# Optimization experiments

Hardware: AMD Instinct MI355X
Metric: run time of the kernel (lower is better)

The kernel has to match this reference:

```python
import jax, jax.numpy as jnp
import numpy as np

N = 5000
NFEAT = 512
NHID = 64
NHEADS = 8
NCLASS = 40
ALPHA = 0.2  # leaky relu slope
NEG_INF = -9e15


def setup_inputs() -> dict:
    key = jax.random.key(0)
    ks = jax.random.split(key, 12)
    x = jax.random.normal(ks[0], (N, NFEAT), dtype=jnp.float32)
    # binary adjacency, ~32 avg degree, with self loops
    adj = (jax.random.uniform(ks[1], (N, N)) < (32.0 / N)).astype(jnp.float32)
    adj = jnp.maximum(adj, jnp.eye(N, dtype=jnp.float32))
    s = 1.0 / np.sqrt(NFEAT)
    W_h = jax.random.uniform(ks[2], (NHEADS, NFEAT, NHID), minval=-s, maxval=s, dtype=jnp.float32)
    a_h = jax.random.uniform(ks[3], (NHEADS, 2 * NHID), minval=-s, maxval=s, dtype=jnp.float32)
    s2 = 1.0 / np.sqrt(NHID * NHEADS)
    W_o = jax.random.uniform(ks[4], (NHID * NHEADS, NHID), minval=-s2, maxval=s2, dtype=jnp.float32)
    a_o = jax.random.uniform(ks[5], (2 * NHID,), minval=-s2, maxval=s2, dtype=jnp.float32)
    s3 = 1.0 / np.sqrt(NHID)
    fc1_w = jax.random.uniform(ks[6], (NHID, 200), minval=-s3, maxval=s3, dtype=jnp.float32)
    fc1_b = jax.random.uniform(ks[7], (200,), minval=-s3, maxval=s3, dtype=jnp.float32)
    s4 = 1.0 / np.sqrt(200)
    fc2_w = jax.random.uniform(ks[8], (200, NCLASS), minval=-s4, maxval=s4, dtype=jnp.float32)
    fc2_b = jax.random.uniform(ks[9], (NCLASS,), minval=-s4, maxval=s4, dtype=jnp.float32)
    return {"x": x, "adj": adj, "W_h": W_h, "a_h": a_h, "W_o": W_o, "a_o": a_o,
            "fc1_w": fc1_w, "fc1_b": fc1_b, "fc2_w": fc2_w, "fc2_b": fc2_b}


def _masked_attention(e, adj):
    # e: [..., N, N]; mask where adj == 0, then row softmax
    e = jnp.where(adj > 0, e, NEG_INF)
    return jax.nn.softmax(e, axis=-1)


def reference(x, adj, W_h, a_h, W_o, a_o, fc1_w, fc1_b, fc2_w, fc2_b):
    # ---- multi-head GAT layer (concat=True), eval mode (dropout off) ----
    Wh = jnp.einsum('nf,hfo->hno', x, W_h)                 # [H, N, nhid]
    f1 = jnp.einsum('hno,ho->hn', Wh, a_h[:, :NHID])       # [H, N]
    f2 = jnp.einsum('hno,ho->hn', Wh, a_h[:, NHID:])       # [H, N]
    e = jax.nn.leaky_relu(f1[:, :, None] + f2[:, None, :], ALPHA)  # [H, N, N]
    att = _masked_attention(e, adj[None, :, :])
    h = jnp.einsum('hnm,hmo->hno', att, Wh)                # [H, N, nhid]
    h1 = jax.nn.elu(h).transpose(1, 0, 2).reshape(N, NHEADS * NHID)  # concat heads

    # ---- output GAT layer (concat=False) ----
    Wh2 = h1 @ W_o                                         # [N, nhid]
    g1 = Wh2 @ a_o[:NHID]                                  # [N]
    g2 = Wh2 @ a_o[NHID:]                                  # [N]
    e2 = jax.nn.leaky_relu(g1[:, None] + g2[None, :], ALPHA)
    att2 = _masked_attention(e2, adj)
    h2 = att2 @ Wh2                                        # [N, nhid]

    # ---- MLP head ----
    h3 = jax.nn.elu(h2 @ fc1_w + fc1_b)
    return h3 @ fc2_w + fc2_b                              # [N, nclass]
```

## Files before the change

kernel.cpp:

```cpp
#include <hip/hip_runtime.h>

typedef unsigned short u16;
typedef unsigned int u32;
typedef unsigned long long u64;
typedef __bf16 bf16_t;
typedef __bf16 bf16x8 __attribute__((ext_vector_type(8)));
typedef u16 u16x8 __attribute__((ext_vector_type(8)));
typedef float f32x4 __attribute__((ext_vector_type(4)));
typedef u32 u32x4 __attribute__((ext_vector_type(4)));

#define NN 5000
#define NF 512
#define NH 64
#define HEADS 8
#define NCLS 40
#define CAP 128
#define LRELU 0.2f

#define BM_BLKS 1250
#define G1_BLKS (79 * HEADS)
#define K1_GRID (BM_BLKS + G1_BLKS)
#define W0_BLKS 64
#define PRM_BLKS 8
#define K0_GRID (W0_BLKS + PRM_BLKS)

__device__ __forceinline__ bool adj_is_bf16(const void* adj) {
    return ((*(const u32*)adj) & 0xFFFFu) != 0u;
}
__device__ __forceinline__ u16 rne_bf16(float f) {
    u32 u = __float_as_uint(f);
    u += 0x7FFFu + ((u >> 16) & 1u);
    return (u16)(u >> 16);
}
__device__ __forceinline__ float up_bf16(u16 h) {
    return __uint_as_float((u32)h << 16);
}
__device__ __forceinline__ float in_f32(const void* p, int idx, bool isb) {
    return isb ? up_bf16(((const u16*)p)[idx]) : ((const float*)p)[idx];
}
__device__ __forceinline__ u32x4 ntload4(const void* p, int idx) {
    return __builtin_nontemporal_load(((const u32x4*)p) + idx);
}
union U8cast { u16x8 u; bf16x8 b; };

__global__ __launch_bounds__(256) void cvt_w(const void* __restrict__ W_h,
                                             const void* __restrict__ adj,
                                             const void* W_o, const void* a_o,
                                             const void* f1w, const void* f1b,
                                             const void* f2w, const void* f2b,
                                             u16* __restrict__ whc,
                                             float* W_oc, float* a_oc,
                                             float* f1wc, float* f1bc,
                                             float* f2wc, float* f2bc) {
    const bool isb = adj_is_bf16(adj);
    const int b = blockIdx.x;
    if (b < W0_BLKS) {
        const int W4 = HEADS * NF * NH / 4;
        for (int iw = b * 256 + threadIdx.x; iw < W4; iw += W0_BLKS * 256) {
            u16 q[4];
            if (isb) {
                ushort4 vv = ((const ushort4*)W_h)[iw];
                q[0] = vv.x; q[1] = vv.y; q[2] = vv.z; q[3] = vv.w;
            } else {
                u32x4 vv = ntload4(W_h, iw);
                q[0] = rne_bf16(__uint_as_float(vv[0])); q[1] = rne_bf16(__uint_as_float(vv[1]));
                q[2] = rne_bf16(__uint_as_float(vv[2])); q[3] = rne_bf16(__uint_as_float(vv[3]));
            }
            const int e0 = iw * 4;
            const int h = e0 >> 15;
            const int rem = e0 & 32767;
            const int f = rem >> 6, o0 = rem & 63;
            const int base = (h * 16 + (f >> 5)) * 2048 + ((f >> 3) & 3) * 128 + (f & 7);
            #pragma unroll
            for (int k = 0; k < 4; ++k) {
                const int o = o0 + k;
                whc[base + (o >> 4) * 512 + (o & 15) * 8] = q[k];
            }
        }
    } else {
        const int s1 = HEADS * NH * NH, s2 = 2 * NH,
                  s3 = NH * 200, s4 = 200, s5 = 200 * NCLS, s6 = NCLS;
        const int total = s1 + s2 + s3 + s4 + s5 + s6;
        const int pb = b - W0_BLKS;
        for (int i = pb * 256 + threadIdx.x; i < total; i += PRM_BLKS * 256) {
            const void* src; float* dst; int off = i;
            if (off < s1) { src = W_o;  dst = W_oc; }
            else if ((off -= s1) < s2) { src = a_o;  dst = a_oc; }
            else if ((off -= s2) < s3) { src = f1w;  dst = f1wc; }
            else if ((off -= s3) < s4) { src = f1b;  dst = f1bc; }
            else if ((off -= s4) < s5) { src = f2w;  dst = f2wc; }
            else { off -= s5;           src = f2b;  dst = f2bc; }
            dst[off] = isb ? up_bf16(((const u16*)src)[off]) : ((const float*)src)[off];
        }
    }
}

__global__ __launch_bounds__(256) void gemm1_f(const void* __restrict__ x,
                                               const bf16_t* __restrict__ Wf,
                                               const void* __restrict__ a_h,
                                               const void* __restrict__ adj,
                                               int* __restrict__ nbr, int* __restrict__ deg,
                                               float* __restrict__ Wh,
                                               float* __restrict__ f1,
                                               float* __restrict__ f2) {
    const bool isb = adj_is_bf16(adj);
    const int lane = threadIdx.x & 63;
    const int wid  = threadIdx.x >> 6;
    const int b = blockIdx.x;

    int aidx = -1, gidx = -1;
    if (b < 1875) {
        const int g = b / 3, r3 = b % 3;
        if (r3 < 2) aidx = 2 * g + r3;
        else        gidx = g;
    } else {
        gidx = 625 + (b - 1875);
    }

    if (aidx >= 0) {
        const int r = aidx * 4 + wid;
        u64 my0 = 0ull, my1 = 0ull;
        if (!isb) {
            const float* row = (const float*)adj + (size_t)r * NN;
            #pragma unroll
            for (int pass = 0; pass < 2; ++pass) {
                u32x4 v[10];
                #pragma unroll
                for (int k = 0; k < 10; ++k) {
                    int c = (pass * 10 + k) * 64 + lane;
                    v[k] = (c < 1250) ? ntload4(row, c) : (u32x4){0u, 0u, 0u, 0u};
                }
                #pragma unroll
                for (int k = 0; k < 10; ++k) {
                    int i = pass * 10 + k;
                    #pragma unroll
                    for (int j = 0; j < 4; ++j) {
                        u64 m = __ballot(v[k][j] != 0u);
                        int w = i * 4 + j;
                        if (w == lane)      my0 = m;
                        if (w == lane + 64) my1 = m;
                    }
                }
            }
        } else {
            const u16* row = (const u16*)adj + (size_t)r * NN;
            u32x4 v[10];
            #pragma unroll
            for (int k = 0; k < 10; ++k) {
                int c = k * 64 + lane;
                v[k] = (c < 625) ? ntload4(row, c) : (u32x4){0u, 0u, 0u, 0u};
            }
            #pragma unroll
            for (int k = 0; k < 10; ++k) {
                #pragma unroll
                for (int j = 0; j < 4; ++j) {
                    u64 mlo = __ballot((v[k][j] & 0xFFFFu) != 0u);
                    u64 mhi = __ballot((v[k][j] >> 16) != 0u);
                    int wl = k * 8 + 2 * j, wh = wl + 1;
                    if (wl == lane)      my0 = mlo;
                    if (wl == lane + 64) my1 = mlo;
                    if (wh == lane)      my0 = mhi;
                    if (wh == lane + 64) my1 = mhi;
                }
            }
        }
        int* nrow = nbr + (size_t)r * CAP;
        int pc = __popcll(my0);
        int scan = pc;
        #pragma unroll
        for (int o = 1; o < 64; o <<= 1) {
            int t2 = __shfl_up(scan, o);
            if (lane >= o) scan += t2;
        }
        int off = scan - pc;
        {
            const int w = lane;
            u64 mw = my0;
            while (mw) {
                int bb = __ffsll(mw) - 1;
                mw &= mw - 1;
                int elem = !isb ? ((w >> 2) * 64 + bb) * 4 + (w & 3)
                                : ((w >> 3) * 64 + bb) * 8 + (w & 7);
                if (off < CAP) nrow[off] = elem;
                ++off;
            }
        }
        const int base = __shfl(scan, 63);
        int pc1 = __popcll(my1);
        int scan1 = pc1;
        #pragma unroll
        for (int o = 1; o < 64; o <<= 1) {
            int t2 = __shfl_up(scan1, o);
            if (lane >= o) scan1 += t2;
        }
        int off1 = base + scan1 - pc1;
        {
            const int w = lane + 64;
            u64 mw = my1;
            while (mw) {
                int bb = __ffsll(mw) - 1;
                mw &= mw - 1;
                int elem = !isb ? ((w >> 2) * 64 + bb) * 4 + (w & 3)
                                : ((w >> 3) * 64 + bb) * 8 + (w & 7);
                if (off1 < CAP) nrow[off1] = elem;
                ++off1;
            }
        }
        const int total = base + __shfl(scan1, 63);
        if (lane == 0) deg[r] = total < CAP ? total : CAP;
        return;
    }

    const int rg = gidx % 79;
    const int h  = gidx / 79;
    const int quad = lane >> 4;
    const int lr   = lane & 15;
    const int kq   = quad * 8;
    const int nCol = wid * 16 + lr;
    __shared__ float f1s[4][64], f2s[4][64];

    const bf16_t* Bf = Wf + (size_t)h * (16 * 2048) + threadIdx.x * 8;
    bf16x8 bfrag[16];
    #pragma unroll
    for (int s = 0; s < 16; ++s) bfrag[s] = *(const bf16x8*)(Bf + s * 2048);

    const float a1c = in_f32(a_h, h * 128 + nCol, isb);
    const float a2c = in_f32(a_h, h * 128 + NH + nCol, isb);

    for (int t = 0; t < 4; ++t) {
        const int rb = rg * 64 + t * 16;
        int row  = rb + lr;
        int rowc = row < NN ? row : NN - 1;
        f32x4 acc = {0.f, 0.f, 0.f, 0.f};
        if (!isb) {
            const float* xp = (const float*)x + (size_t)rowc * NF + kq;
            #pragma unroll
            for (int s = 0; s < 16; ++s) {
                float4 lo = *(const float4*)(xp + s * 32);
                float4 hi = *(const float4*)(xp + s * 32 + 4);
                bf16x8 a;
                a[0] = (bf16_t)lo.x; a[1] = (bf16_t)lo.y; a[2] = (bf16_t)lo.z; a[3] = (bf16_t)lo.w;
                a[4] = (bf16_t)hi.x; a[5] = (bf16_t)hi.y; a[6] = (bf16_t)hi.z; a[7] = (bf16_t)hi.w;
                acc = __builtin_amdgcn_mfma_f32_16x16x32_bf16(a, bfrag[s], acc, 0, 0, 0);
            }
        } else {
            const u16* xp = (const u16*)x + (size_t)rowc * NF + kq;
            #pragma unroll
            for (int s = 0; s < 16; ++s) {
                U8cast cc;
                cc.u = *(const u16x8*)(xp + s * 32);
                acc = __builtin_amdgcn_mfma_f32_16x16x32_bf16(cc.b, bfrag[s], acc, 0, 0, 0);
            }
        }
        #pragma unroll
        for (int r = 0; r < 4; ++r) {
            int gr = rb + quad * 4 + r;
            if (gr < NN) Wh[(size_t)gr * (HEADS * NH) + h * NH + nCol] = acc[r];
            float p1 = acc[r] * a1c, p2 = acc[r] * a2c;
            #pragma unroll
            for (int o = 8; o; o >>= 1) { p1 += __shfl_xor(p1, o); p2 += __shfl_xor(p2, o); }
            if (lr == 0) { f1s[wid][t * 16 + quad * 4 + r] = p1; f2s[wid][t * 16 + quad * 4 + r] = p2; }
        }
    }
    __syncthreads();
    if (wid == 0) {
        int gr = rg * 64 + lane;
        if (gr < NN) {
            f1[h * NN + gr] = f1s[0][lane] + f1s[1][lane] + f1s[2][lane] + f1s[3][lane];
            f2[h * NN + gr] = f2s[0][lane] + f2s[1][lane] + f2s[2][lane] + f2s[3][lane];
        }
    }
}

__global__ __launch_bounds__(256) void agg1f(const int* __restrict__ nbr,
                                             const int* __restrict__ deg,
                                             const float* __restrict__ Wh,
                                             const float* __restrict__ f1,
                                             const float* __restrict__ f2,
                                             float* __restrict__ h1) {
    const int lane = threadIdx.x & 63;
    const int wid  = threadIdx.x >> 6;
    const int n = blockIdx.x;
    __shared__ int s_nbr[CAP];
    __shared__ float s_p[8][CAP];
    const int d = deg[n];
    for (int i = threadIdx.x; i < d; i += 256) s_nbr[i] = nbr[(size_t)n * CAP + i];
    __syncthreads();

    const int ha = wid, hb = wid + 4;
    const int nb0 = (lane < d) ? s_nbr[lane] : 0;
    const int nb1 = (lane + 64 < d) ? s_nbr[lane + 64] : 0;
    const float f10 = f1[ha * NN + n], f11 = f1[hb * NN + n];
    const float* f2ha = f2 + (size_t)ha * NN;
    const float* f2hb = f2 + (size_t)hb * NN;

    float e00 = -INFINITY, e01 = -INFINITY, e10 = -INFINITY, e11 = -INFINITY;
    if (lane < d) {
        float a = f10 + f2ha[nb0]; e00 = a > 0.f ? a : LRELU * a;
        float b = f11 + f2hb[nb0]; e10 = b > 0.f ? b : LRELU * b;
    }
    if (lane + 64 < d) {
        float a = f10 + f2ha[nb1]; e01 = a > 0.f ? a : LRELU * a;
        float b = f11 + f2hb[nb1]; e11 = b > 0.f ? b : LRELU * b;
    }
    float mx0 = fmaxf(e00, e01), mx1 = fmaxf(e10, e11);
    #pragma unroll
    for (int o = 32; o; o >>= 1) {
        mx0 = fmaxf(mx0, __shfl_xor(mx0, o));
        mx1 = fmaxf(mx1, __shfl_xor(mx1, o));
    }
    float p00 = lane < d ? expf(e00 - mx0) : 0.f;
    float p01 = lane + 64 < d ? expf(e01 - mx0) : 0.f;
    float p10 = lane < d ? expf(e10 - mx1) : 0.f;
    float p11 = lane + 64 < d ? expf(e11 - mx1) : 0.f;
    float sm0 = p00 + p01, sm1 = p10 + p11;
    #pragma unroll
    for (int o = 32; o; o >>= 1) { sm0 += __shfl_xor(sm0, o); sm1 += __shfl_xor(sm1, o); }

    const float i0 = 1.f / sm0, i1 = 1.f / sm1;
    s_p[ha][lane] = p00 * i0; s_p[ha][lane + 64] = p01 * i0;
    s_p[hb][lane] = p10 * i1; s_p[hb][lane + 64] = p11 * i1;
    __syncthreads();

    const float* ap = s_p[2 * wid + (lane >> 5)];
    const float* wp = Wh + wid * 128 + 2 * lane;
    float A0x = 0.f, A0y = 0.f, A1x = 0.f, A1y = 0.f;
    float A2x = 0.f, A2y = 0.f, A3x = 0.f, A3y = 0.f;
    int j = 0;
    for (; j + 8 <= d; j += 8) {
        #pragma unroll
        for (int u = 0; u < 8; ++u) {
            const float2 v = *(const float2*)(wp + (size_t)s_nbr[j + u] * (HEADS * NH));
            const float a = ap[j + u];
            if ((u & 3) == 0)      { A0x += a * v.x; A0y += a * v.y; }
            else if ((u & 3) == 1) { A1x += a * v.x; A1y += a * v.y; }
            else if ((u & 3) == 2) { A2x += a * v.x; A2y += a * v.y; }
            else                   { A3x += a * v.x; A3y += a * v.y; }
        }
    }
    for (; j < d; ++j) {
        const float2 v = *(const float2*)(wp + (size_t)s_nbr[j] * (HEADS * NH));
        const float a = ap[j];
        A0x += a * v.x; A0y += a * v.y;
    }
    float hx = A0x + A1x + A2x + A3x;
    float hy = A0y + A1y + A2y + A3y;
    hx = hx > 0.f ? hx : expf(hx) - 1.f;
    hy = hy > 0.f ? hy : expf(hy) - 1.f;
    *(float2*)(h1 + (size_t)n * (HEADS * NH) + wid * 128 + 2 * lane) = make_float2(hx, hy);
}

__global__ __launch_bounds__(256) void gemm2_4(const float* __restrict__ h1,
                                               const float* __restrict__ W_o,
                                               const float* __restrict__ a_o,
                                               float* __restrict__ Wh2,
                                               float* __restrict__ g1,
                                               float* __restrict__ g2) {
    const int t = threadIdx.x;
    const int n0 = blockIdx.x * 4;
    __shared__ float sh[4 * 512];
    __shared__ float ps[4][4][64];
    const float4* src = (const float4*)(h1 + (size_t)n0 * 512);
    ((float4*)sh)[t]       = src[t];
    ((float4*)sh)[t + 256] = src[t + 256];
    __syncthreads();
    const int o = t & 63, part = t >> 6;
    float a0 = 0.f, a1 = 0.f, a2 = 0.f, a3 = 0.f;
    const float* wo = W_o + part * 128 * 64 + o;
    const float* s0 = sh + part * 128;
    #pragma unroll 4
    for (int f = 0; f < 128; ++f) {
        float w = wo[f * 64];
        a0 += s0[f] * w; a1 += s0[512 + f] * w; a2 += s0[1024 + f] * w; a3 += s0[1536 + f] * w;
    }
    ps[part][0][o] = a0; ps[part][1][o] = a1; ps[part][2][o] = a2; ps[part][3][o] = a3;
    __syncthreads();
    const int nd = t >> 6;
    float w2 = ps[0][nd][o] + ps[1][nd][o] + ps[2][nd][o] + ps[3][nd][o];
    Wh2[(size_t)(n0 + nd) * 64 + o] = w2;
    float p1 = w2 * a_o[o], p2 = w2 * a_o[64 + o];
    #pragma unroll
    for (int s = 32; s; s >>= 1) { p1 += __shfl_xor(p1, s); p2 += __shfl_xor(p2, s); }
    if (o == 0) { g1[n0 + nd] = p1; g2[n0 + nd] = p2; }
}

__global__ __launch_bounds__(256) void agg2_mlp(const float* __restrict__ Wh2,
                                                const float* __restrict__ g1,
                                                const float* __restrict__ g2,
                                                const int* __restrict__ nbr,
                                                const int* __restrict__ deg,
                                                const float* __restrict__ fc1_w,
                                                const float* __restrict__ fc1_b,
                                                const float* __restrict__ fc2_w,
                                                const float* __restrict__ fc2_b,
                                                float* __restrict__ out) {
    const int lane = threadIdx.x & 63;
    const int wid  = threadIdx.x >> 6;
    const int t = threadIdx.x;
    const int n0 = blockIdx.x * 4;
    const int n = n0 + wid;
    __shared__ float s_alpha[4][CAP];
    __shared__ int   s_nbr[4][CAP];
    __shared__ float s_h2[4][NH];
    __shared__ float s_h3[4][200];
    __shared__ float ps2[2][4][NCLS];
    const int d = deg[n];
    const int* nb = nbr + (size_t)n * CAP;
    const float gn = g1[n];

    float mx = -INFINITY;
    for (int j = lane; j < d; j += 64) {
        int m = nb[j];
        s_nbr[wid][j] = m;
        float e = gn + g2[m];
        e = e > 0.f ? e : LRELU * e;
        s_alpha[wid][j] = e;
        mx = fmaxf(mx, e);
    }
    #pragma unroll
    for (int o = 32; o; o >>= 1) mx = fmaxf(mx, __shfl_xor(mx, o));
    float sm = 0.f;
    for (int j = lane; j < d; j += 64) {
        float p = expf(s_alpha[wid][j] - mx);
        s_alpha[wid][j] = p;
        sm += p;
    }
    #pragma unroll
    for (int o = 32; o; o >>= 1) sm += __shfl_xor(sm, o);

    float acc0 = 0.f, acc1 = 0.f, acc2 = 0.f, acc3 = 0.f;
    int j = 0;
    for (; j + 4 <= d; j += 4) {
        acc0 += s_alpha[wid][j]     * Wh2[(size_t)s_nbr[wid][j]     * NH + lane];
        acc1 += s_alpha[wid][j + 1] * Wh2[(size_t)s_nbr[wid][j + 1] * NH + lane];
        acc2 += s_alpha[wid][j + 2] * Wh2[(size_t)s_nbr[wid][j + 2] * NH + lane];
        acc3 += s_alpha[wid][j + 3] * Wh2[(size_t)s_nbr[wid][j + 3] * NH + lane];
    }
    for (; j < d; ++j) acc0 += s_alpha[wid][j] * Wh2[(size_t)s_nbr[wid][j] * NH + lane];
    s_h2[wid][lane] = (acc0 + acc1 + acc2 + acc3) / sm;
    __syncthreads();

    if (t < 200) {
        float b0 = 0.f, b1 = 0.f, b2 = 0.f, b3 = 0.f;
        #pragma unroll 4
        for (int f = 0; f < NH; ++f) {
            float w = fc1_w[f * 200 + t];
            b0 += s_h2[0][f] * w; b1 += s_h2[1][f] * w; b2 += s_h2[2][f] * w; b3 += s_h2[3][f] * w;
        }
        float bb = fc1_b[t];
        b0 += bb; b1 += bb; b2 += bb; b3 += bb;
        s_h3[0][t] = b0 > 0.f ? b0 : expf(b0) - 1.f;
        s_h3[1][t] = b1 > 0.f ? b1 : expf(b1) - 1.f;
        s_h3[2][t] = b2 > 0.f ? b2 : expf(b2) - 1.f;
        s_h3[3][t] = b3 > 0.f ? b3 : expf(b3) - 1.f;
    }
    __syncthreads();

    if (t < 80) {
        const int o = t % 40, fh = t / 40;
        float c0 = 0.f, c1 = 0.f, c2 = 0.f, c3 = 0.f;
        #pragma unroll 4
        for (int f = fh * 100; f < fh * 100 + 100; ++f) {
            float w = fc2_w[f * NCLS + o];
            c0 += s_h3[0][f] * w; c1 += s_h3[1][f] * w; c2 += s_h3[2][f] * w; c3 += s_h3[3][f] * w;
        }
        ps2[fh][0][o] = c0; ps2[fh][1][o] = c1; ps2[fh][2][o] = c2; ps2[fh][3][o] = c3;
    }
    __syncthreads();
    if (t < 160) {
        const int nd = t / 40, o = t % 40;
        out[(size_t)(n0 + nd) * NCLS + o] = ps2[0][nd][o] + ps2[1][nd][o] + fc2_b[o];
    }
}

extern "C" void kernel_launch(void* const* d_in, const int* in_sizes, int n_in,
                              void* d_out, int out_size, void* d_ws, size_t ws_size,
                              hipStream_t stream) {
    const void* x     = d_in[0];
    const void* adj   = d_in[1];
    const void* W_h   = d_in[2];
    const void* a_h   = d_in[3];
    const void* W_o   = d_in[4];
    const void* a_o   = d_in[5];
    const void* fc1_w = d_in[6];
    const void* fc1_b = d_in[7];
    const void* fc2_w = d_in[8];
    const void* fc2_b = d_in[9];
    float* out = (float*)d_out;

    char* ws = (char*)d_ws;
    int*   nbr   = (int*)(ws + 0);
    int*   deg   = (int*)(ws + 2560000);
    float* Wh    = (float*)(ws + 2580000);
    float* f1    = (float*)(ws + 12820000);
    float* f2    = (float*)(ws + 12980000);
    float* h1    = (float*)(ws + 13140000);
    float* Wh2   = (float*)(ws + 23380000);
    float* g1    = (float*)(ws + 24660000);
    float* g2    = (float*)(ws + 24680000);
    float* W_oc  = (float*)(ws + 24700000);
    float* a_oc  = (float*)(ws + 24831072);
    float* f1wc  = (float*)(ws + 24831584);
    float* f1bc  = (float*)(ws + 24882784);
    float* f2wc  = (float*)(ws + 24883584);
    float* f2bc  = (float*)(ws + 24915584);
    u16*   whc   = (u16*)(ws + 24915744);

    cvt_w<<<K0_GRID, 256, 0, stream>>>(W_h, adj, W_o, a_o, fc1_w, fc1_b, fc2_w, fc2_b,
                                       whc, W_oc, a_oc, f1wc, f1bc, f2wc, f2bc);
    gemm1_f<<<K1_GRID, 256, 0, stream>>>(x, (const bf16_t*)whc, a_h, adj,
                                         nbr, deg, Wh, f1, f2);
    agg1f<<<NN, 256, 0, stream>>>(nbr, deg, Wh, f1, f2, h1);
    gemm2_4<<<NN / 4, 256, 0, stream>>>(h1, W_oc, a_oc, Wh2, g1, g2);
    agg2_mlp<<<NN / 4, 256, 0, stream>>>(Wh2, g1, g2, nbr, deg,
                                         f1wc, f1bc, f2wc, f2bc, out);
}
```

Before: 301.8 us.

## Split adjacency row scan across two waves and reorder GEMM-first block layout

The adjacency-to-neighbor-list pass now assigns each row to two waves, each scanning half the columns. Their counts are combined through shared memory and a block barrier, where before one wave made two passes over the whole row. The adjacency blocks now come after the GEMM blocks in the grid instead of being interleaved in a 2:1 pattern. The aim is more memory-level parallelism and shorter per-wave latency on the bandwidth-bound adjacency read, at the cost of a __syncthreads and twice as many adjacency blocks.

```diff
diff --git a/kernel.cpp b/kernel.cpp
--- a/kernel.cpp
+++ b/kernel.cpp
@@ -17,9 +17,9 @@
 #define CAP 128
 #define LRELU 0.2f
 
-#define BM_BLKS 1250
 #define G1_BLKS (79 * HEADS)
-#define K1_GRID (BM_BLKS + G1_BLKS)
+#define ADJ_BLKS 2500
+#define K1_GRID (G1_BLKS + ADJ_BLKS)
 #define W0_BLKS 64
 #define PRM_BLKS 8
 #define K0_GRID (W0_BLKS + PRM_BLKS)
@@ -103,121 +103,91 @@
                                                float* __restrict__ Wh,
                                                float* __restrict__ f1,
                                                float* __restrict__ f2) {
-    const bool isb = adj_is_bf16(adj);
     const int lane = threadIdx.x & 63;
     const int wid  = threadIdx.x >> 6;
     const int b = blockIdx.x;
-
-    int aidx = -1, gidx = -1;
-    if (b < 1875) {
-        const int g = b / 3, r3 = b % 3;
-        if (r3 < 2) aidx = 2 * g + r3;
-        else        gidx = g;
-    } else {
-        gidx = 625 + (b - 1875);
-    }
-
-    if (aidx >= 0) {
-        const int r = aidx * 4 + wid;
-        u64 my0 = 0ull, my1 = 0ull;
+    __shared__ float f1s[4][64], f2s[4][64];
+    __shared__ int s_cnt[4];
+
+    if (b >= G1_BLKS) {
+        const bool isb = adj_is_bf16(adj);
+        const int a = b - G1_BLKS;
+        const int r = a * 2 + (wid >> 1);
+        const int hf = wid & 1;
+        u64 myw = 0ull;
         if (!isb) {
             const float* row = (const float*)adj + (size_t)r * NN;
-            #pragma unroll
-            for (int pass = 0; pass < 2; ++pass) {
-                u32x4 v[10];
+            u32x4 v[10];
+            #pragma unroll
+            for (int k = 0; k < 10; ++k) {
+                int c = hf * 640 + k * 64 + lane;
+                v[k] = (c < 1250) ? ntload4(row, c) : (u32x4){0u, 0u, 0u, 0u};
+            }
+            #pragma unroll
+            for (int k = 0; k < 10; ++k) {
                 #pragma unroll
-                for (int k = 0; k < 10; ++k) {
-                    int c = (pass * 10 + k) * 64 + lane;
-                    v[k] = (c < 1250) ? ntload4(row, c) : (u32x4){0u, 0u, 0u, 0u};
-                }
-                #pragma unroll
-                for (int k = 0; k < 10; ++k) {
-                    int i = pass * 10 + k;
-                    #pragma unroll
-                    for (int j = 0; j < 4; ++j) {
-                        u64 m = __ballot(v[k][j] != 0u);
-                        int w = i * 4 + j;
-                        if (w == lane)      my0 = m;
-                        if (w == lane + 64) my1 = m;
-                    }
+                for (int j = 0; j < 4; ++j) {
+                    u64 m = __ballot(v[k][j] != 0u);
+                    if (k * 4 + j == lane) myw = m;
                 }
             }
         } else {
             const u16* row = (const u16*)adj + (size_t)r * NN;
-            u32x4 v[10];
-            #pragma unroll
-            for (int k = 0; k < 10; ++k) {
-                int c = k * 64 + lane;
+            u32x4 v[5];
+            #pragma unroll
+            for (int k = 0; k < 5; ++k) {
+                int c = hf * 320 + k * 64 + lane;
                 v[k] = (c < 625) ? ntload4(row, c) : (u32x4){0u, 0u, 0u, 0u};
             }
             #pragma unroll
-            for (int k = 0; k < 10; ++k) {
+            for (int k = 0; k < 5; ++k) {
                 #pragma unroll
                 for (int j = 0; j < 4; ++j) {
                     u64 mlo = __ballot((v[k][j] & 0xFFFFu) != 0u);
                     u64 mhi = __ballot((v[k][j] >> 16) != 0u);
-                    int wl = k * 8 + 2 * j, wh = wl + 1;
-                    if (wl == lane)      my0 = mlo;
-                    if (wl == lane + 64) my1 = mlo;
-                    if (wh == lane)      my0 = mhi;
-                    if (wh == lane + 64) my1 = mhi;
+                    int wl = k * 8 + 2 * j;
+                    if (wl == lane)     myw = mlo;
+                    if (wl + 1 == lane) myw = mhi;
                 }
             }
         }
-        int* nrow = nbr + (size_t)r * CAP;
-        int pc = __popcll(my0);
+        int pc = __popcll(myw);
         int scan = pc;
         #pragma unroll
         for (int o = 1; o < 64; o <<= 1) {
             int t2 = __shfl_up(scan, o);
             if (lane >= o) scan += t2;
         }
-        int off = scan - pc;
-        {
-            const int w = lane;
-            u64 mw = my0;
-            while (mw) {
-                int bb = __ffsll(mw) - 1;
-                mw &= mw - 1;
-                int elem = !isb ? ((w >> 2) * 64 + bb) * 4 + (w & 3)
-                                : ((w >> 3) * 64 + bb) * 8 + (w & 7);
-                if (off < CAP) nrow[off] = elem;
-                ++off;
-            }
-        }
-        const int base = __shfl(scan, 63);
-        int pc1 = __popcll(my1);
-        int scan1 = pc1;
-        #pragma unroll
-        for (int o = 1; o < 64; o <<= 1) {
-            int t2 = __shfl_up(scan1, o);
-            if (lane >= o) scan1 += t2;
-        }
-        int off1 = base + scan1 - pc1;
-        {
-            const int w = lane + 64;
-            u64 mw = my1;
-            while (mw) {
-                int bb = __ffsll(mw) - 1;
-                mw &= mw - 1;
-                int elem = !isb ? ((w >> 2) * 64 + bb) * 4 + (w & 3)
-                                : ((w >> 3) * 64 + bb) * 8 + (w & 7);
-                if (off1 < CAP) nrow[off1] = elem;
-                ++off1;
-            }
-        }
-        const int total = base + __shfl(scan1, 63);
-        if (lane == 0) deg[r] = total < CAP ? total : CAP;
+        const int cnt = __shfl(scan, 63);
+        if (lane == 0) s_cnt[wid] = cnt;
+        __syncthreads();
+        const int base0 = hf ? s_cnt[wid - 1] : 0;
+        int off = base0 + scan - pc;
+        int* nrow = nbr + (size_t)r * CAP;
+        const int w = hf * 40 + lane;
+        u64 mw = myw;
+        while (mw) {
+            int bb = __ffsll(mw) - 1;
+            mw &= mw - 1;
+            int elem = !isb ? ((w >> 2) * 64 + bb) * 4 + (w & 3)
+                            : ((w >> 3) * 64 + bb) * 8 + (w & 7);
+            if (off < CAP) nrow[off] = elem;
+            ++off;
+        }
+        if (hf == 1 && lane == 0) {
+            int tot = base0 + cnt;
+            deg[r] = tot < CAP ? tot : CAP;
+        }
         return;
     }
 
-    const int rg = gidx % 79;
-    const int h  = gidx / 79;
+    const bool isb = adj_is_bf16(adj);
+    const int rg = b % 79;
+    const int h  = b / 79;
     const int quad = lane >> 4;
     const int lr   = lane & 15;
     const int kq   = quad * 8;
     const int nCol = wid * 16 + lr;
-    __shared__ float f1s[4][64], f2s[4][64];
 
     const bf16_t* Bf = Wf + (size_t)h * (16 * 2048) + threadIdx.x * 8;
     bf16x8 bfrag[16];
```

Result: faster. 282.7 us (-6.3%).
